# Kernel optimization log

Hardware: AMD Instinct MI355X
Metric: run time of the kernel (lower is better)

## Reference

```python
import jax, jax.numpy as jnp
import numpy as np

LN_EPS = 1e-5


def setup_inputs() -> dict:
    key = jax.random.key(0)
    ks = jax.random.split(key, 5)
    N, C, R = 200000, 256, 8
    x = jax.random.normal(ks[0], (N, C), dtype=jnp.float32)
    w1 = jax.random.normal(ks[1], (C // R, C), dtype=jnp.float32) * (1.0 / np.sqrt(C))
    w2 = jax.random.normal(ks[2], (C, C // R), dtype=jnp.float32) * (1.0 / np.sqrt(C // R))
    conv_w = jax.random.normal(ks[3], (1, 2, 3), dtype=jnp.float32) * 0.4
    ln_g = jnp.ones((C,), dtype=jnp.float32)
    ln_b = jnp.zeros((C,), dtype=jnp.float32)
    gamma = jax.random.normal(ks[4], (1,), dtype=jnp.float32)
    return {"x": x, "w1": w1, "w2": w2, "conv_w": conv_w,
            "ln_g": ln_g, "ln_b": ln_b, "gamma": gamma}


def _mlp(v, w1, w2):
    # torch Linear: y = v @ W^T ; ReLU between
    return jnp.maximum(v @ w1.T, 0.0) @ w2.T


def reference(x, w1, w2, conv_w, ln_g, ln_b, gamma):
    # ---- channel attention: pool over nodes (dim 0) -> [C] ----
    avg = jnp.mean(x, axis=0)
    mx = jnp.max(x, axis=0)
    att_c = jax.nn.sigmoid(_mlp(avg, w1, w2) + _mlp(mx, w1, w2))  # [C]
    xc = x * att_c  # broadcast over nodes

    # ---- spatial attention over nodes ----
    mu = jnp.mean(xc, axis=1, keepdims=True)
    var = jnp.var(xc, axis=1, keepdims=True)
    xn = (xc - mu) * jax.lax.rsqrt(var + LN_EPS) * ln_g + ln_b  # LayerNorm [N,C]
    a = jnp.mean(xn, axis=1)  # [N]
    m = jnp.max(xn, axis=1)   # [N]
    y = jnp.stack([a, m], axis=0)[None]  # [1, 2, N]
    z = jax.lax.conv_general_dilated(
        y, conv_w, window_strides=(1,), padding=[(1, 1)],
        dimension_numbers=("NCW", "OIW", "NCW"))  # [1, 1, N]
    s = jax.nn.sigmoid(z[0, 0])[:, None]  # [N, 1]

    return xc + gamma * (xc * s)
```

## Files before the change

### kernel.cpp

```cpp
#include <hip/hip_runtime.h>
#include <hip/hip_bf16.h>
#include <math.h>

#define CCH 256
#define ABLK 1024
#define A2BLK 16
#define ROWS 64

typedef float floatx4 __attribute__((ext_vector_type(4)));

__device__ __forceinline__ float wred_sum(float v) {
#pragma unroll
  for (int m = 32; m; m >>= 1) v += __shfl_xor(v, m, 64);
  return v;
}

__global__ __launch_bounds__(256) void k_colred(
    const float4* __restrict__ x4, float* __restrict__ psum,
    float* __restrict__ pmax, int N) {
  const int lane = threadIdx.x & 63;
  const int sr = threadIdx.x >> 6;
  float4 s = make_float4(0.f, 0.f, 0.f, 0.f);
  float4 m = make_float4(-INFINITY, -INFINITY, -INFINITY, -INFINITY);
  for (int r = blockIdx.x * 4 + sr; r < N; r += gridDim.x * 4) {
    float4 v = x4[(size_t)r * 64 + lane];
    s.x += v.x; s.y += v.y; s.z += v.z; s.w += v.w;
    m.x = fmaxf(m.x, v.x); m.y = fmaxf(m.y, v.y);
    m.z = fmaxf(m.z, v.z); m.w = fmaxf(m.w, v.w);
  }
  __shared__ float4 ls[256], lm[256];
  ls[threadIdx.x] = s; lm[threadIdx.x] = m;
  __syncthreads();
  if (threadIdx.x < 64) {
    float4 s0 = ls[lane], s1 = ls[64 + lane], s2 = ls[128 + lane], s3 = ls[192 + lane];
    float4 m0 = lm[lane], m1 = lm[64 + lane], m2 = lm[128 + lane], m3 = lm[192 + lane];
    float4 so, mo;
    so.x = (s0.x + s1.x) + (s2.x + s3.x);
    so.y = (s0.y + s1.y) + (s2.y + s3.y);
    so.z = (s0.z + s1.z) + (s2.z + s3.z);
    so.w = (s0.w + s1.w) + (s2.w + s3.w);
    mo.x = fmaxf(fmaxf(m0.x, m1.x), fmaxf(m2.x, m3.x));
    mo.y = fmaxf(fmaxf(m0.y, m1.y), fmaxf(m2.y, m3.y));
    mo.z = fmaxf(fmaxf(m0.z, m1.z), fmaxf(m2.z, m3.z));
    mo.w = fmaxf(fmaxf(m0.w, m1.w), fmaxf(m2.w, m3.w));
    ((float4*)psum)[(size_t)blockIdx.x * 64 + lane] = so;
    ((float4*)pmax)[(size_t)blockIdx.x * 64 + lane] = mo;
  }
}

__global__ __launch_bounds__(256) void k_colred2(
    const float* __restrict__ psum, const float* __restrict__ pmax,
    float* __restrict__ s2sum, float* __restrict__ s2max) {
  const int lane = threadIdx.x & 63;
  const int sr = threadIdx.x >> 6;
  const int base = blockIdx.x * (ABLK / A2BLK);
  float4 s = make_float4(0.f, 0.f, 0.f, 0.f);
  float4 m = make_float4(-INFINITY, -INFINITY, -INFINITY, -INFINITY);
  for (int p = base + sr; p < base + (ABLK / A2BLK); p += 4) {
    float4 v = ((const float4*)psum)[(size_t)p * 64 + lane];
    s.x += v.x; s.y += v.y; s.z += v.z; s.w += v.w;
    float4 w = ((const float4*)pmax)[(size_t)p * 64 + lane];
    m.x = fmaxf(m.x, w.x); m.y = fmaxf(m.y, w.y);
    m.z = fmaxf(m.z, w.z); m.w = fmaxf(m.w, w.w);
  }
  __shared__ float4 ls[256], lm[256];
  ls[threadIdx.x] = s; lm[threadIdx.x] = m;
  __syncthreads();
  if (threadIdx.x < 64) {
    float4 s0 = ls[lane], s1 = ls[64 + lane], s2 = ls[128 + lane], s3 = ls[192 + lane];
    float4 m0 = lm[lane], m1 = lm[64 + lane], m2 = lm[128 + lane], m3 = lm[192 + lane];
    float4 so, mo;
    so.x = (s0.x + s1.x) + (s2.x + s3.x);
    so.y = (s0.y + s1.y) + (s2.y + s3.y);
    so.z = (s0.z + s1.z) + (s2.z + s3.z);
    so.w = (s0.w + s1.w) + (s2.w + s3.w);
    mo.x = fmaxf(fmaxf(m0.x, m1.x), fmaxf(m2.x, m3.x));
    mo.y = fmaxf(fmaxf(m0.y, m1.y), fmaxf(m2.y, m3.y));
    mo.z = fmaxf(fmaxf(m0.z, m1.z), fmaxf(m2.z, m3.z));
    mo.w = fmaxf(fmaxf(m0.w, m1.w), fmaxf(m2.w, m3.w));
    ((float4*)s2sum)[(size_t)blockIdx.x * 64 + lane] = so;
    ((float4*)s2max)[(size_t)blockIdx.x * 64 + lane] = mo;
  }
}

__global__ __launch_bounds__(256) void k_att(
    const float* __restrict__ s2sum, const float* __restrict__ s2max,
    const float* __restrict__ w1, const float* __restrict__ w2,
    float* __restrict__ att, int N) {
  __shared__ float vec[2][CCH];
  __shared__ float hid[2][32];
  __shared__ float4 ls[256], lm[256];
  const int tid = threadIdx.x;
  const int lane = tid & 63;
  const int sr = tid >> 6;
  float4 s = make_float4(0.f, 0.f, 0.f, 0.f);
  float4 m = make_float4(-INFINITY, -INFINITY, -INFINITY, -INFINITY);
  for (int p = sr; p < A2BLK; p += 4) {
    float4 v = ((const float4*)s2sum)[(size_t)p * 64 + lane];
    s.x += v.x; s.y += v.y; s.z += v.z; s.w += v.w;
    float4 w = ((const float4*)s2max)[(size_t)p * 64 + lane];
    m.x = fmaxf(m.x, w.x); m.y = fmaxf(m.y, w.y);
    m.z = fmaxf(m.z, w.z); m.w = fmaxf(m.w, w.w);
  }
  ls[tid] = s; lm[tid] = m;
  __syncthreads();
  if (tid < 64) {
    float4 s0 = ls[lane], s1 = ls[64 + lane], s2 = ls[128 + lane], s3 = ls[192 + lane];
    float4 m0 = lm[lane], m1 = lm[64 + lane], m2 = lm[128 + lane], m3 = lm[192 + lane];
    float inv = 1.f / (float)N;
    vec[0][4 * lane + 0] = ((s0.x + s1.x) + (s2.x + s3.x)) * inv;
    vec[0][4 * lane + 1] = ((s0.y + s1.y) + (s2.y + s3.y)) * inv;
    vec[0][4 * lane + 2] = ((s0.z + s1.z) + (s2.z + s3.z)) * inv;
    vec[0][4 * lane + 3] = ((s0.w + s1.w) + (s2.w + s3.w)) * inv;
    vec[1][4 * lane + 0] = fmaxf(fmaxf(m0.x, m1.x), fmaxf(m2.x, m3.x));
    vec[1][4 * lane + 1] = fmaxf(fmaxf(m0.y, m1.y), fmaxf(m2.y, m3.y));
    vec[1][4 * lane + 2] = fmaxf(fmaxf(m0.z, m1.z), fmaxf(m2.z, m3.z));
    vec[1][4 * lane + 3] = fmaxf(fmaxf(m0.w, m1.w), fmaxf(m2.w, m3.w));
  }
  __syncthreads();
  if (tid < 64) {
    const int which = tid >> 5;
    const int j = tid & 31;
    float acc = 0.f;
    for (int c = 0; c < CCH; ++c) acc += vec[which][c] * w1[j * CCH + c];
    hid[which][j] = fmaxf(acc, 0.f);
  }
  __syncthreads();
  {
    const int c = tid;
    float acc = 0.f;
#pragma unroll
    for (int j = 0; j < 32; ++j) acc += (hid[0][j] + hid[1][j]) * w2[c * 32 + j];
    att[c] = 1.f / (1.f + expf(-acc));
  }
}

__global__ __launch_bounds__(256) void k_fused(
    const float4* __restrict__ x4, const float* __restrict__ att,
    const float* __restrict__ ln_g, const float* __restrict__ ln_b,
    const float* __restrict__ conv_w, const float* __restrict__ gamma,
    float4* __restrict__ out4, int N) {
  const int lane = threadIdx.x & 63;
  const int wid = threadIdx.x >> 6;
  const float4 ac = ((const float4*)att)[lane];
  const float4 g4 = ((const float4*)ln_g)[lane];
  const float4 b4 = ((const float4*)ln_b)[lane];
  float cw0 = conv_w[0], cw1 = conv_w[1], cw2 = conv_w[2];
  float cw3 = conv_w[3], cw4 = conv_w[4], cw5 = conv_w[5];
  const float gm = gamma[0];
  __shared__ float a_s[ROWS + 2], m_s[ROWS + 2];
  const int r0 = blockIdx.x * ROWS;

  for (int i = wid; i < ROWS + 2; i += 4) {
    const int gr = r0 - 1 + i;
    float asum = 0.f, amax = 0.f;
    if (gr >= 0 && gr < N) {
      float4 v = x4[(size_t)gr * 64 + lane];
      v.x *= ac.x; v.y *= ac.y; v.z *= ac.z; v.w *= ac.w;
      float rsum = (v.x + v.y) + (v.z + v.w);
      rsum = wred_sum(rsum);
      const float mu = rsum * (1.f / 256.f);
      const float dx = v.x - mu, dy = v.y - mu, dz = v.z - mu, dw = v.w - mu;
      float ssq = (dx * dx + dy * dy) + (dz * dz + dw * dw);
      ssq = wred_sum(ssq);
      const float rs = rsqrtf(ssq * (1.f / 256.f) + 1e-5f);
      const float n0 = dx * rs * g4.x + b4.x;
      const float n1 = dy * rs * g4.y + b4.y;
      const float n2 = dz * rs * g4.z + b4.z;
      const float n3 = dw * rs * g4.w + b4.w;
      float xs = (n0 + n1) + (n2 + n3);
      float xm = fmaxf(fmaxf(n0, n1), fmaxf(n2, n3));
#pragma unroll
      for (int msk = 32; msk; msk >>= 1) {
        xs += __shfl_xor(xs, msk, 64);
        xm = fmaxf(xm, __shfl_xor(xm, msk, 64));
      }
      asum = xs * (1.f / 256.f);
      amax = xm;
    }
    if (lane == 0) { a_s[i] = asum; m_s[i] = amax; }
  }
  __syncthreads();

  for (int i = wid; i < ROWS; i += 4) {
    const int gr = r0 + i;
    if (gr >= N) break;
    const float z = a_s[i] * cw0 + a_s[i + 1] * cw1 + a_s[i + 2] * cw2 +
                    m_s[i] * cw3 + m_s[i + 1] * cw4 + m_s[i + 2] * cw5;
    const float sg = 1.f / (1.f + expf(-z));
    const float scale = 1.f + gm * sg;
    float4 v = x4[(size_t)gr * 64 + lane];
    floatx4 o;
    o.x = v.x * ac.x * scale;
    o.y = v.y * ac.y * scale;
    o.z = v.z * ac.z * scale;
    o.w = v.w * ac.w * scale;
    __builtin_nontemporal_store(o, (floatx4*)&out4[(size_t)gr * 64 + lane]);
  }
}

extern "C" void kernel_launch(void* const* d_in, const int* in_sizes, int n_in,
                              void* d_out, int out_size, void* d_ws, size_t ws_size,
                              hipStream_t stream) {
  const float* x = (const float*)d_in[0];
  const float* w1 = (const float*)d_in[1];
  const float* w2 = (const float*)d_in[2];
  const float* conv_w = (const float*)d_in[3];
  const float* ln_g = (const float*)d_in[4];
  const float* ln_b = (const float*)d_in[5];
  const float* gamma = (const float*)d_in[6];
  float* out = (float*)d_out;
  const int N = in_sizes[0] / CCH;

  float* psum = (float*)d_ws;
  float* pmax = psum + (size_t)ABLK * CCH;
  float* s2sum = pmax + (size_t)ABLK * CCH;
  float* s2max = s2sum + (size_t)A2BLK * CCH;
  float* att = s2max + (size_t)A2BLK * CCH;

  k_colred<<<ABLK, 256, 0, stream>>>((const float4*)x, psum, pmax, N);
  k_colred2<<<A2BLK, 256, 0, stream>>>(psum, pmax, s2sum, s2max);
  k_att<<<1, 256, 0, stream>>>(s2sum, s2max, w1, w2, att, N);
  const int cblocks = (N + ROWS - 1) / ROWS;
  k_fused<<<cblocks, 256, 0, stream>>>((const float4*)x, att, ln_g, ln_b,
                                       conv_w, gamma, (float4*)out, N);
}
```

Baseline: 429.6 us.

## Fuse all stages into one cooperative kernel with grid-wide syncs

Replaces the four separate launches (column reduction, second-stage reduction, attention MLP, fused normalize/output) with a single cooperative kernel of 1024 blocks separated by grid syncs. Block 0 alone reduces the partial sums and computes the channel attention, while the other blocks wait at the second grid sync. Each block then handles a contiguous chunk of about 196 rows instead of 64, so the halo rows reloaded per block are amortized. This removes launch gaps and intermediate buffers, but adds grid-sync cost and a serial single-block phase, and the fixed 256-entry shared arrays cap the chunk size.

```diff
diff --git a/kernel.cpp b/kernel.cpp
--- a/kernel.cpp
+++ b/kernel.cpp
@@ -1,11 +1,12 @@
 #include <hip/hip_runtime.h>
-#include <hip/hip_bf16.h>
+#include <hip/hip_cooperative_groups.h>
 #include <math.h>
 
+namespace cg = cooperative_groups;
+
 #define CCH 256
-#define ABLK 1024
-#define A2BLK 16
-#define ROWS 64
+#define GBLK 1024
+#define THR 256
 
 typedef float floatx4 __attribute__((ext_vector_type(4)));
 
@@ -15,213 +16,180 @@
   return v;
 }
 
-__global__ __launch_bounds__(256) void k_colred(
-    const float4* __restrict__ x4, float* __restrict__ psum,
-    float* __restrict__ pmax, int N) {
-  const int lane = threadIdx.x & 63;
-  const int sr = threadIdx.x >> 6;
-  float4 s = make_float4(0.f, 0.f, 0.f, 0.f);
-  float4 m = make_float4(-INFINITY, -INFINITY, -INFINITY, -INFINITY);
-  for (int r = blockIdx.x * 4 + sr; r < N; r += gridDim.x * 4) {
-    float4 v = x4[(size_t)r * 64 + lane];
-    s.x += v.x; s.y += v.y; s.z += v.z; s.w += v.w;
-    m.x = fmaxf(m.x, v.x); m.y = fmaxf(m.y, v.y);
-    m.z = fmaxf(m.z, v.z); m.w = fmaxf(m.w, v.w);
+__global__ __launch_bounds__(THR, 4) void k_all(
+    const float4* __restrict__ x4,
+    const float* __restrict__ w1, const float* __restrict__ w2,
+    const float* __restrict__ conv_w,
+    const float* __restrict__ ln_g, const float* __restrict__ ln_b,
+    const float* __restrict__ gamma,
+    float* __restrict__ psum, float* __restrict__ pmax,
+    float* __restrict__ att, float4* __restrict__ out4, int N) {
+  const int tid  = threadIdx.x;
+  const int lane = tid & 63;
+  const int wid  = tid >> 6;
+  const int bid  = blockIdx.x;
+
+  __shared__ float4 ls[THR], lm[THR];
+
+  {
+    float4 s = make_float4(0.f, 0.f, 0.f, 0.f);
+    float4 m = make_float4(-INFINITY, -INFINITY, -INFINITY, -INFINITY);
+    for (int r = bid * 4 + wid; r < N; r += GBLK * 4) {
+      float4 v = x4[(size_t)r * 64 + lane];
+      s.x += v.x; s.y += v.y; s.z += v.z; s.w += v.w;
+      m.x = fmaxf(m.x, v.x); m.y = fmaxf(m.y, v.y);
+      m.z = fmaxf(m.z, v.z); m.w = fmaxf(m.w, v.w);
+    }
+    ls[tid] = s; lm[tid] = m;
+    __syncthreads();
+    if (tid < 64) {
+      float4 s0 = ls[lane], s1 = ls[64 + lane], s2 = ls[128 + lane], s3 = ls[192 + lane];
+      float4 m0 = lm[lane], m1 = lm[64 + lane], m2 = lm[128 + lane], m3 = lm[192 + lane];
+      float4 so, mo;
+      so.x = (s0.x + s1.x) + (s2.x + s3.x);
+      so.y = (s0.y + s1.y) + (s2.y + s3.y);
+      so.z = (s0.z + s1.z) + (s2.z + s3.z);
+      so.w = (s0.w + s1.w) + (s2.w + s3.w);
+      mo.x = fmaxf(fmaxf(m0.x, m1.x), fmaxf(m2.x, m3.x));
+      mo.y = fmaxf(fmaxf(m0.y, m1.y), fmaxf(m2.y, m3.y));
+      mo.z = fmaxf(fmaxf(m0.z, m1.z), fmaxf(m2.z, m3.z));
+      mo.w = fmaxf(fmaxf(m0.w, m1.w), fmaxf(m2.w, m3.w));
+      ((float4*)psum)[(size_t)bid * 64 + lane] = so;
+      ((float4*)pmax)[(size_t)bid * 64 + lane] = mo;
+    }
+    __threadfence();
   }
-  __shared__ float4 ls[256], lm[256];
-  ls[threadIdx.x] = s; lm[threadIdx.x] = m;
-  __syncthreads();
-  if (threadIdx.x < 64) {
-    float4 s0 = ls[lane], s1 = ls[64 + lane], s2 = ls[128 + lane], s3 = ls[192 + lane];
-    float4 m0 = lm[lane], m1 = lm[64 + lane], m2 = lm[128 + lane], m3 = lm[192 + lane];
-    float4 so, mo;
-    so.x = (s0.x + s1.x) + (s2.x + s3.x);
-    so.y = (s0.y + s1.y) + (s2.y + s3.y);
-    so.z = (s0.z + s1.z) + (s2.z + s3.z);
-    so.w = (s0.w + s1.w) + (s2.w + s3.w);
-    mo.x = fmaxf(fmaxf(m0.x, m1.x), fmaxf(m2.x, m3.x));
-    mo.y = fmaxf(fmaxf(m0.y, m1.y), fmaxf(m2.y, m3.y));
-    mo.z = fmaxf(fmaxf(m0.z, m1.z), fmaxf(m2.z, m3.z));
-    mo.w = fmaxf(fmaxf(m0.w, m1.w), fmaxf(m2.w, m3.w));
-    ((float4*)psum)[(size_t)blockIdx.x * 64 + lane] = so;
-    ((float4*)pmax)[(size_t)blockIdx.x * 64 + lane] = mo;
+  cg::this_grid().sync();
+
+  if (bid == 0) {
+    __shared__ float vec[2][CCH];
+    __shared__ float hid[2][32];
+    {
+      float4 s = make_float4(0.f, 0.f, 0.f, 0.f);
+      float4 m = make_float4(-INFINITY, -INFINITY, -INFINITY, -INFINITY);
+      for (int b = wid; b < GBLK; b += 4) {
+        float4 v = ((const float4*)psum)[(size_t)b * 64 + lane];
+        s.x += v.x; s.y += v.y; s.z += v.z; s.w += v.w;
+        float4 w = ((const float4*)pmax)[(size_t)b * 64 + lane];
+        m.x = fmaxf(m.x, w.x); m.y = fmaxf(m.y, w.y);
+        m.z = fmaxf(m.z, w.z); m.w = fmaxf(m.w, w.w);
+      }
+      ls[tid] = s; lm[tid] = m;
+      __syncthreads();
+      if (tid < 64) {
+        float4 s0 = ls[lane], s1 = ls[64 + lane], s2 = ls[128 + lane], s3 = ls[192 + lane];
+        float4 m0 = lm[lane], m1 = lm[64 + lane], m2 = lm[128 + lane], m3 = lm[192 + lane];
+        const float inv = 1.f / (float)N;
+        vec[0][4 * lane + 0] = ((s0.x + s1.x) + (s2.x + s3.x)) * inv;
+        vec[0][4 * lane + 1] = ((s0.y + s1.y) + (s2.y + s3.y)) * inv;
+        vec[0][4 * lane + 2] = ((s0.z + s1.z) + (s2.z + s3.z)) * inv;
+        vec[0][4 * lane + 3] = ((s0.w + s1.w) + (s2.w + s3.w)) * inv;
+        vec[1][4 * lane + 0] = fmaxf(fmaxf(m0.x, m1.x), fmaxf(m2.x, m3.x));
+        vec[1][4 * lane + 1] = fmaxf(fmaxf(m0.y, m1.y), fmaxf(m2.y, m3.y));
+        vec[1][4 * lane + 2] = fmaxf(fmaxf(m0.z, m1.z), fmaxf(m2.z, m3.z));
+        vec[1][4 * lane + 3] = fmaxf(fmaxf(m0.w, m1.w), fmaxf(m2.w, m3.w));
+      }
+      __syncthreads();
+      if (tid < 64) {
+        const int which = tid >> 5;
+        const int j = tid & 31;
+        float acc = 0.f;
+        for (int c = 0; c < CCH; ++c) acc += vec[which][c] * w1[j * CCH + c];
+        hid[which][j] = fmaxf(acc, 0.f);
+      }
+      __syncthreads();
+      {
+        float acc = 0.f;
+#pragma unroll
+        for (int j = 0; j < 32; ++j) acc += (hid[0][j] + hid[1][j]) * w2[tid * 32 + j];
+        att[tid] = 1.f / (1.f + expf(-acc));
+      }
+    }
+    __threadfence();
   }
-}
+  cg::this_grid().sync();
 
-__global__ __launch_bounds__(256) void k_colred2(
-    const float* __restrict__ psum, const float* __restrict__ pmax,
-    float* __restrict__ s2sum, float* __restrict__ s2max) {
-  const int lane = threadIdx.x & 63;
-  const int sr = threadIdx.x >> 6;
-  const int base = blockIdx.x * (ABLK / A2BLK);
-  float4 s = make_float4(0.f, 0.f, 0.f, 0.f);
-  float4 m = make_float4(-INFINITY, -INFINITY, -INFINITY, -INFINITY);
-  for (int p = base + sr; p < base + (ABLK / A2BLK); p += 4) {
-    float4 v = ((const float4*)psum)[(size_t)p * 64 + lane];
-    s.x += v.x; s.y += v.y; s.z += v.z; s.w += v.w;
-    float4 w = ((const float4*)pmax)[(size_t)p * 64 + lane];
-    m.x = fmaxf(m.x, w.x); m.y = fmaxf(m.y, w.y);
-    m.z = fmaxf(m.z, w.z); m.w = fmaxf(m.w, w.w);
-  }
-  __shared__ float4 ls[256], lm[256];
-  ls[threadIdx.x] = s; lm[threadIdx.x] = m;
-  __syncthreads();
-  if (threadIdx.x < 64) {
-    float4 s0 = ls[lane], s1 = ls[64 + lane], s2 = ls[128 + lane], s3 = ls[192 + lane];
-    float4 m0 = lm[lane], m1 = lm[64 + lane], m2 = lm[128 + lane], m3 = lm[192 + lane];
-    float4 so, mo;
-    so.x = (s0.x + s1.x) + (s2.x + s3.x);
-    so.y = (s0.y + s1.y) + (s2.y + s3.y);
-    so.z = (s0.z + s1.z) + (s2.z + s3.z);
-    so.w = (s0.w + s1.w) + (s2.w + s3.w);
-    mo.x = fmaxf(fmaxf(m0.x, m1.x), fmaxf(m2.x, m3.x));
-    mo.y = fmaxf(fmaxf(m0.y, m1.y), fmaxf(m2.y, m3.y));
-    mo.z = fmaxf(fmaxf(m0.z, m1.z), fmaxf(m2.z, m3.z));
-    mo.w = fmaxf(fmaxf(m0.w, m1.w), fmaxf(m2.w, m3.w));
-    ((float4*)s2sum)[(size_t)blockIdx.x * 64 + lane] = so;
-    ((float4*)s2max)[(size_t)blockIdx.x * 64 + lane] = mo;
-  }
-}
+  {
+    const int chunk = (N + GBLK - 1) / GBLK;
+    const int r0 = bid * chunk;
+    const int rows = (N - r0 < chunk) ? (N - r0) : chunk;
+    __shared__ float a_s[256], m_s[256];
+    if (rows > 0) {
+      const float4 ac = ((const float4*)att)[lane];
+      const float4 g4 = ((const float4*)ln_g)[lane];
+      const float4 b4 = ((const float4*)ln_b)[lane];
+      const float cw0 = conv_w[0], cw1 = conv_w[1], cw2 = conv_w[2];
+      const float cw3 = conv_w[3], cw4 = conv_w[4], cw5 = conv_w[5];
+      const float gm = gamma[0];
 
-__global__ __launch_bounds__(256) void k_att(
-    const float* __restrict__ s2sum, const float* __restrict__ s2max,
-    const float* __restrict__ w1, const float* __restrict__ w2,
-    float* __restrict__ att, int N) {
-  __shared__ float vec[2][CCH];
-  __shared__ float hid[2][32];
-  __shared__ float4 ls[256], lm[256];
-  const int tid = threadIdx.x;
-  const int lane = tid & 63;
-  const int sr = tid >> 6;
-  float4 s = make_float4(0.f, 0.f, 0.f, 0.f);
-  float4 m = make_float4(-INFINITY, -INFINITY, -INFINITY, -INFINITY);
-  for (int p = sr; p < A2BLK; p += 4) {
-    float4 v = ((const float4*)s2sum)[(size_t)p * 64 + lane];
-    s.x += v.x; s.y += v.y; s.z += v.z; s.w += v.w;
-    float4 w = ((const float4*)s2max)[(size_t)p * 64 + lane];
-    m.x = fmaxf(m.x, w.x); m.y = fmaxf(m.y, w.y);
-    m.z = fmaxf(m.z, w.z); m.w = fmaxf(m.w, w.w);
-  }
-  ls[tid] = s; lm[tid] = m;
-  __syncthreads();
-  if (tid < 64) {
-    float4 s0 = ls[lane], s1 = ls[64 + lane], s2 = ls[128 + lane], s3 = ls[192 + lane];
-    float4 m0 = lm[lane], m1 = lm[64 + lane], m2 = lm[128 + lane], m3 = lm[192 + lane];
-    float inv = 1.f / (float)N;
-    vec[0][4 * lane + 0] = ((s0.x + s1.x) + (s2.x + s3.x)) * inv;
-    vec[0][4 * lane + 1] = ((s0.y + s1.y) + (s2.y + s3.y)) * inv;
-    vec[0][4 * lane + 2] = ((s0.z + s1.z) + (s2.z + s3.z)) * inv;
-    vec[0][4 * lane + 3] = ((s0.w + s1.w) + (s2.w + s3.w)) * inv;
-    vec[1][4 * lane + 0] = fmaxf(fmaxf(m0.x, m1.x), fmaxf(m2.x, m3.x));
-    vec[1][4 * lane + 1] = fmaxf(fmaxf(m0.y, m1.y), fmaxf(m2.y, m3.y));
-    vec[1][4 * lane + 2] = fmaxf(fmaxf(m0.z, m1.z), fmaxf(m2.z, m3.z));
-    vec[1][4 * lane + 3] = fmaxf(fmaxf(m0.w, m1.w), fmaxf(m2.w, m3.w));
-  }
-  __syncthreads();
-  if (tid < 64) {
-    const int which = tid >> 5;
-    const int j = tid & 31;
-    float acc = 0.f;
-    for (int c = 0; c < CCH; ++c) acc += vec[which][c] * w1[j * CCH + c];
-    hid[which][j] = fmaxf(acc, 0.f);
-  }
-  __syncthreads();
-  {
-    const int c = tid;
-    float acc = 0.f;
+      for (int i = wid; i < rows + 2; i += 4) {
+        const int gr = r0 - 1 + i;
+        float asum = 0.f, amax = 0.f;
+        if (gr >= 0 && gr < N) {
+          float4 v = x4[(size_t)gr * 64 + lane];
+          v.x *= ac.x; v.y *= ac.y; v.z *= ac.z; v.w *= ac.w;
+          float rsum = (v.x + v.y) + (v.z + v.w);
+          rsum = wred_sum(rsum);
+          const float mu = rsum * (1.f / 256.f);
+          const float dx = v.x - mu, dy = v.y - mu, dz = v.z - mu, dw = v.w - mu;
+          float ssq = (dx * dx + dy * dy) + (dz * dz + dw * dw);
+          ssq = wred_sum(ssq);
+          const float rs = rsqrtf(ssq * (1.f / 256.f) + 1e-5f);
+          const float n0 = dx * rs * g4.x + b4.x;
+          const float n1 = dy * rs * g4.y + b4.y;
+          const float n2 = dz * rs * g4.z + b4.z;
+          const float n3 = dw * rs * g4.w + b4.w;
+          float xs = (n0 + n1) + (n2 + n3);
+          float xm = fmaxf(fmaxf(n0, n1), fmaxf(n2, n3));
 #pragma unroll
-    for (int j = 0; j < 32; ++j) acc += (hid[0][j] + hid[1][j]) * w2[c * 32 + j];
-    att[c] = 1.f / (1.f + expf(-acc));
-  }
-}
+          for (int msk = 32; msk; msk >>= 1) {
+            xs += __shfl_xor(xs, msk, 64);
+            xm = fmaxf(xm, __shfl_xor(xm, msk, 64));
+          }
+          asum = xs * (1.f / 256.f);
+          amax = xm;
+        }
+        if (lane == 0) { a_s[i] = asum; m_s[i] = amax; }
+      }
+      __syncthreads();
 
-__global__ __launch_bounds__(256) void k_fused(
-    const float4* __restrict__ x4, const float* __restrict__ att,
-    const float* __restrict__ ln_g, const float* __restrict__ ln_b,
-    const float* __restrict__ conv_w, const float* __restrict__ gamma,
-    float4* __restrict__ out4, int N) {
-  const int lane = threadIdx.x & 63;
-  const int wid = threadIdx.x >> 6;
-  const float4 ac = ((const float4*)att)[lane];
-  const float4 g4 = ((const float4*)ln_g)[lane];
-  const float4 b4 = ((const float4*)ln_b)[lane];
-  float cw0 = conv_w[0], cw1 = conv_w[1], cw2 = conv_w[2];
-  float cw3 = conv_w[3], cw4 = conv_w[4], cw5 = conv_w[5];
-  const float gm = gamma[0];
-  __shared__ float a_s[ROWS + 2], m_s[ROWS + 2];
-  const int r0 = blockIdx.x * ROWS;
-
-  for (int i = wid; i < ROWS + 2; i += 4) {
-    const int gr = r0 - 1 + i;
-    float asum = 0.f, amax = 0.f;
-    if (gr >= 0 && gr < N) {
-      float4 v = x4[(size_t)gr * 64 + lane];
-      v.x *= ac.x; v.y *= ac.y; v.z *= ac.z; v.w *= ac.w;
-      float rsum = (v.x + v.y) + (v.z + v.w);
-      rsum = wred_sum(rsum);
-      const float mu = rsum * (1.f / 256.f);
-      const float dx = v.x - mu, dy = v.y - mu, dz = v.z - mu, dw = v.w - mu;
-      float ssq = (dx * dx + dy * dy) + (dz * dz + dw * dw);
-      ssq = wred_sum(ssq);
-      const float rs = rsqrtf(ssq * (1.f / 256.f) + 1e-5f);
-      const float n0 = dx * rs * g4.x + b4.x;
-      const float n1 = dy * rs * g4.y + b4.y;
-      const float n2 = dz * rs * g4.z + b4.z;
-      const float n3 = dw * rs * g4.w + b4.w;
-      float xs = (n0 + n1) + (n2 + n3);
-      float xm = fmaxf(fmaxf(n0, n1), fmaxf(n2, n3));
-#pragma unroll
-      for (int msk = 32; msk; msk >>= 1) {
-        xs += __shfl_xor(xs, msk, 64);
-        xm = fmaxf(xm, __shfl_xor(xm, msk, 64));
+      for (int i = wid; i < rows; i += 4) {
+        const int gr = r0 + i;
+        const float z = a_s[i] * cw0 + a_s[i + 1] * cw1 + a_s[i + 2] * cw2 +
+                        m_s[i] * cw3 + m_s[i + 1] * cw4 + m_s[i + 2] * cw5;
+        const float sg = 1.f / (1.f + expf(-z));
+        const float scale = 1.f + gm * sg;
+        float4 v = x4[(size_t)gr * 64 + lane];
+        floatx4 o;
+        o.x = v.x * ac.x * scale;
+        o.y = v.y * ac.y * scale;
+        o.z = v.z * ac.z * scale;
+        o.w = v.w * ac.w * scale;
+        __builtin_nontemporal_store(o, (floatx4*)&out4[(size_t)gr * 64 + lane]);
       }
-      asum = xs * (1.f / 256.f);
-      amax = xm;
     }
-    if (lane == 0) { a_s[i] = asum; m_s[i] = amax; }
-  }
-  __syncthreads();
-
-  for (int i = wid; i < ROWS; i += 4) {
-    const int gr = r0 + i;
-    if (gr >= N) break;
-    const float z = a_s[i] * cw0 + a_s[i + 1] * cw1 + a_s[i + 2] * cw2 +
-                    m_s[i] * cw3 + m_s[i + 1] * cw4 + m_s[i + 2] * cw5;
-    const float sg = 1.f / (1.f + expf(-z));
-    const float scale = 1.f + gm * sg;
-    float4 v = x4[(size_t)gr * 64 + lane];
-    floatx4 o;
-    o.x = v.x * ac.x * scale;
-    o.y = v.y * ac.y * scale;
-    o.z = v.z * ac.z * scale;
-    o.w = v.w * ac.w * scale;
-    __builtin_nontemporal_store(o, (floatx4*)&out4[(size_t)gr * 64 + lane]);
   }
 }
 
 extern "C" void kernel_launch(void* const* d_in, const int* in_sizes, int n_in,
                               void* d_out, int out_size, void* d_ws, size_t ws_size,
                               hipStream_t stream) {
-  const float* x = (const float*)d_in[0];
-  const float* w1 = (const float*)d_in[1];
-  const float* w2 = (const float*)d_in[2];
-  const float* conv_w = (const float*)d_in[3];
-  const float* ln_g = (const float*)d_in[4];
-  const float* ln_b = (const float*)d_in[5];
-  const float* gamma = (const float*)d_in[6];
-  float* out = (float*)d_out;
-  const int N = in_sizes[0] / CCH;
+  const float4* x4p   = (const float4*)d_in[0];
+  const float* w1p    = (const float*)d_in[1];
+  const float* w2p    = (const float*)d_in[2];
+  const float* cwp    = (const float*)d_in[3];
+  const float* lngp   = (const float*)d_in[4];
+  const float* lnbp   = (const float*)d_in[5];
+  const float* gmp    = (const float*)d_in[6];
+  float4* outp        = (float4*)d_out;
+  int N = in_sizes[0] / CCH;
 
   float* psum = (float*)d_ws;
-  float* pmax = psum + (size_t)ABLK * CCH;
-  float* s2sum = pmax + (size_t)ABLK * CCH;
-  float* s2max = s2sum + (size_t)A2BLK * CCH;
-  float* att = s2max + (size_t)A2BLK * CCH;
+  float* pmax = psum + (size_t)GBLK * CCH;
+  float* attp = pmax + (size_t)GBLK * CCH;
 
-  k_colred<<<ABLK, 256, 0, stream>>>((const float4*)x, psum, pmax, N);
-  k_colred2<<<A2BLK, 256, 0, stream>>>(psum, pmax, s2sum, s2max);
-  k_att<<<1, 256, 0, stream>>>(s2sum, s2max, w1, w2, att, N);
-  const int cblocks = (N + ROWS - 1) / ROWS;
-  k_fused<<<cblocks, 256, 0, stream>>>((const float4*)x, att, ln_g, ln_b,
-                                       conv_w, gamma, (float4*)out, N);
+  void* args[] = {(void*)&x4p, (void*)&w1p, (void*)&w2p, (void*)&cwp,
+                  (void*)&lngp, (void*)&lnbp, (void*)&gmp,
+                  (void*)&psum, (void*)&pmax, (void*)&attp, (void*)&outp, (void*)&N};
+  hipLaunchCooperativeKernel((void*)k_all, dim3(GBLK), dim3(THR), args, 0, stream);
 }
```

New measurement: 750.3 us. +74.6%, slower.
